# Optimization experiments

Measured on AMD Instinct MI355X. Metric: run time of the kernel, lower is better.

## Reference

```python
import jax, jax.numpy as jnp
import numpy as np

IN_DIM = 256
OUT_DIM = 256
GRID_SIZE = 8
K = 3  # spline_order
LOW, UP = -1.0, 1.0
BATCH = 512


def _control_grid():
    # equally spaced control points, extended by K on each side (paper sec 2.4)
    spacing = (UP - LOW) / GRID_SIZE
    g = jnp.arange(-K, GRID_SIZE + K + 1, dtype=jnp.float32) * spacing + LOW
    # buffer shape (out_dim, in_dim, G + 2K + 1)
    return jnp.broadcast_to(g[None, None, :], (OUT_DIM, IN_DIM, g.shape[0]))


def _bspline_bases(x, grid):
    # x: (B, in_dim); grid: (out, in, T). Cox-de Boor recursion.
    xx = x[:, None, :, None]          # (B, 1, in, 1)
    g = grid[None]                    # (1, out, in, T)
    # order-0 (piecewise-constant) bases
    b = ((xx >= g[..., :-1]) & (xx < g[..., 1:])).astype(x.dtype)
    for j in range(1, K + 1):
        b = (xx - g[..., :-(j + 1)]) / (g[..., j:-1] - g[..., :-(j + 1)]) * b[..., :-1] \
          + (g[..., j + 1:] - xx) / (g[..., j + 1:] - g[..., 1:-j]) * b[..., 1:]
    return b  # (B, out, in, G + K)


def setup_inputs() -> dict:
    key = jax.random.key(0)
    k1, k2, k3 = jax.random.split(key, 3)
    x = jax.random.normal(k1, (BATCH, IN_DIM), dtype=jnp.float32)
    # xavier_normal_ on (out, in, G+K): fan_in = in*(G+K) -> std = sqrt(2/(fan_in+fan_out))
    fan_out = IN_DIM * (GRID_SIZE + K)  # torch convention: dim0 = fan_out, rest = fan_in
    fan_in = OUT_DIM * (GRID_SIZE + K)
    std = float(np.sqrt(2.0 / (fan_in + fan_out)))
    coef = jax.random.normal(k2, (OUT_DIM, IN_DIM, GRID_SIZE + K), dtype=jnp.float32) * std
    residual_weight = jax.random.normal(k3, (OUT_DIM, IN_DIM), dtype=jnp.float32) * 0.1
    univariate_weight = jnp.ones((OUT_DIM, IN_DIM), dtype=jnp.float32)
    return {"x": x, "coef": coef, "residual_weight": residual_weight,
            "univariate_weight": univariate_weight}


def reference(x, coef, residual_weight, univariate_weight):
    grid = _control_grid()
    bases = _bspline_bases(x, grid)                      # (B, out, in, G+K)
    spline = jnp.einsum('boig,oig->boi', bases, coef)    # sum over grid dim
    phi = residual_weight[None, :, :] * jax.nn.silu(x)[:, None, :] \
        + univariate_weight[None, :, :] * spline          # (B, out, in)
    return jnp.sum(phi, axis=-1)                          # (B, out)
```

## Files before the change

kernel.cpp:

```cpp
#include <hip/hip_runtime.h>
#include <hip/hip_bf16.h>

typedef unsigned short ushort_t;
typedef unsigned int uint_t;
typedef __attribute__((ext_vector_type(8))) short short8;
typedef __attribute__((ext_vector_type(4))) float f32x4;

#define IN_DIM 256
#define OUT_DIM 256
#define BATCH 512
#define NSPL 11
#define KSLOT 12
#define KDIM (IN_DIM * KSLOT)
#define BKU 384
#define NCHUNK 8

__device__ __forceinline__ uint_t pk2(float lo, float hi) {
  __hip_bfloat162 h = __float22bfloat162_rn(make_float2(lo, hi));
  union { __hip_bfloat162 h2; uint_t u; } c; c.h2 = h;
  return c.u;
}

__global__ __launch_bounds__(256) void build_aw(const float* __restrict__ x,
                                                const float* __restrict__ coef,
                                                const float* __restrict__ rw,
                                                const float* __restrict__ uw,
                                                ushort_t* __restrict__ A,
                                                ushort_t* __restrict__ W) {
  __shared__ float rowc[IN_DIM * NSPL];
  const int bx = blockIdx.x;
  const int t = threadIdx.x;

  if (bx < BATCH) {
    const float xf = x[bx * IN_DIM + t];
    const float tt = (xf + 1.75f) * 4.0f;
    const float fJ = floorf(tt);
    const int J = (int)fJ;
    const float u = tt - fJ;
    const float u2 = u * u, u3 = u2 * u, um = 1.0f - u;
    const float n0 = um * um * um * (1.0f / 6.0f);
    const float n1 = 0.5f * u3 - u2 + (4.0f / 6.0f);
    const float n2 = -0.5f * u3 + 0.5f * u2 + 0.5f * u + (1.0f / 6.0f);
    const float n3 = u3 * (1.0f / 6.0f);
    const float silu = xf / (1.0f + __expf(-xf));

    float v[12];
#pragma unroll
    for (int g = 0; g < NSPL; ++g) {
      float val = 0.0f;
      val = (J == g + 3) ? n0 : val;
      val = (J == g + 2) ? n1 : val;
      val = (J == g + 1) ? n2 : val;
      val = (J == g    ) ? n3 : val;
      v[g] = val;
    }
    v[11] = silu;

    uint_t* dst = (uint_t*)(A + (size_t)bx * KDIM + t * KSLOT);
#pragma unroll
    for (int j = 0; j < 6; ++j) dst[j] = pk2(v[2 * j], v[2 * j + 1]);
  } else {
    const int o = bx - BATCH;
    const float* src = coef + (size_t)o * IN_DIM * NSPL;
#pragma unroll
    for (int j = 0; j < 11; ++j) rowc[t + j * 256] = src[t + j * 256];
    __syncthreads();

    const float us = uw[o * IN_DIM + t];
    const float r  = rw[o * IN_DIM + t];
    const float* c = &rowc[t * NSPL];
    uint_t* dst = (uint_t*)(W + (size_t)o * KDIM + t * KSLOT);
    dst[0] = pk2(us * c[0], us * c[1]);
    dst[1] = pk2(us * c[2], us * c[3]);
    dst[2] = pk2(us * c[4], us * c[5]);
    dst[3] = pk2(us * c[6], us * c[7]);
    dst[4] = pk2(us * c[8], us * c[9]);
    dst[5] = pk2(us * c[10], r);
  }
}

__global__ __launch_bounds__(256, 3) void gemm(const ushort_t* __restrict__ A,
                                               const ushort_t* __restrict__ W,
                                               float* __restrict__ out) {
  __shared__ __attribute__((aligned(16))) ushort_t As[2][16 * BKU];
  __shared__ __attribute__((aligned(16))) ushort_t Ws[2][16 * BKU];
  __shared__ f32x4 red[3][64];

  const int tid = threadIdx.x;
  const int lane = tid & 63;
  const int w = tid >> 6;
  const int B = blockIdx.x;
  const int mt = B >> 4;
  const int nt = ((B & 7) << 1) | ((B >> 3) & 1);
  const int b0 = mt * 16, o0 = nt * 16;
  const int mn = lane & 15;
  const int klane = (lane >> 4) * 8;

  int srcOff[3], ldsOff[3];
#pragma unroll
  for (int i = 0; i < 3; ++i) {
    const int F = ((w * 3 + i) * 64 + lane) * 8;
    const int rowi = F / BKU;
    const int coli = F % BKU;
    srcOff[i] = rowi * KDIM + coli;
    ldsOff[i] = rowi * BKU + (coli ^ ((rowi & 7) << 3));
  }
  const ushort_t* Ap = A + (size_t)b0 * KDIM;
  const ushort_t* Wp = W + (size_t)o0 * KDIM;

  const int mrow = mn * BKU;
  const int msw = (mn & 7) << 3;

  f32x4 acc = {0.f, 0.f, 0.f, 0.f};
  short8 sa0, sa1, sa2, sw0, sw1, sw2;

#define ISSUE(C)                                                              \
  {                                                                           \
    const int kb = (C) * BKU;                                                 \
    sa0 = *(const short8*)(Ap + srcOff[0] + kb);                              \
    sa1 = *(const short8*)(Ap + srcOff[1] + kb);                              \
    sa2 = *(const short8*)(Ap + srcOff[2] + kb);                              \
    sw0 = *(const short8*)(Wp + srcOff[0] + kb);                              \
    sw1 = *(const short8*)(Wp + srcOff[1] + kb);                              \
    sw2 = *(const short8*)(Wp + srcOff[2] + kb);                              \
  }

#define COMMIT(BUF)                                                           \
  {                                                                           \
    *(short8*)&As[BUF][ldsOff[0]] = sa0;                                      \
    *(short8*)&As[BUF][ldsOff[1]] = sa1;                                      \
    *(short8*)&As[BUF][ldsOff[2]] = sa2;                                      \
    *(short8*)&Ws[BUF][ldsOff[0]] = sw0;                                      \
    *(short8*)&Ws[BUF][ldsOff[1]] = sw1;                                      \
    *(short8*)&Ws[BUF][ldsOff[2]] = sw2;                                      \
  }

  ISSUE(0)
  COMMIT(0)
  __syncthreads();

  for (int c = 0; c < NCHUNK; ++c) {
    const int cur = c & 1;

    if (c + 1 < NCHUNK) { ISSUE(c + 1) }

#pragma unroll
    for (int q = 0; q < 3; ++q) {
      const int kidx = w * 96 + q * 32 + klane;
      const int idx = mrow + (kidx ^ msw);
      short8 af  = *(const short8*)&As[cur][idx];
      short8 bfr = *(const short8*)&Ws[cur][idx];
      acc = __builtin_amdgcn_mfma_f32_16x16x32_bf16(af, bfr, acc, 0, 0, 0);
    }

    if (c + 1 < NCHUNK) { COMMIT(cur ^ 1) }
    __syncthreads();
  }

  if (w > 0) red[w - 1][lane] = acc;
  __syncthreads();

  if (w == 0) {
    const f32x4 t0 = red[0][lane];
    const f32x4 t1 = red[1][lane];
    const f32x4 t2 = red[2][lane];
#pragma unroll
    for (int q = 0; q < 4; ++q) acc[q] += t0[q] + t1[q] + t2[q];

    const int col = o0 + mn;
    const int rbase = b0 + (lane >> 4) * 4;
#pragma unroll
    for (int r = 0; r < 4; ++r) {
      out[(size_t)(rbase + r) * OUT_DIM + col] = acc[r];
    }
  }
}

extern "C" void kernel_launch(void* const* d_in, const int* in_sizes, int n_in,
                              void* d_out, int out_size, void* d_ws, size_t ws_size,
                              hipStream_t stream) {
  const float* x    = (const float*)d_in[0];
  const float* coef = (const float*)d_in[1];
  const float* rw   = (const float*)d_in[2];
  const float* uw   = (const float*)d_in[3];
  float* out = (float*)d_out;

  ushort_t* A = (ushort_t*)d_ws;
  ushort_t* W = A + (size_t)BATCH * KDIM;

  build_aw<<<BATCH + OUT_DIM, 256, 0, stream>>>(x, coef, rw, uw, A, W);
  gemm<<<512, 256, 0, stream>>>(A, W, out);
}
```

Measured before the change: 17.86 us.

## Fuse B-spline basis construction into GEMM A-tile packing in LDS

Removes the global A matrix (spline bases plus SiLU per batch row). The GEMM kernel now reads x directly, evaluates the cubic B-spline weights and SiLU, and writes them swizzled into the shared-memory A tile. The W stream is double-buffered through two register sets with an unrolled two-phase loop. This saves a global write and read of the large bf16 A matrix, at the cost of recomputing bases in every column-tile block and extra scattered LDS stores. Out-of-range basis writes go to a dump area in the reduction buffer.

```diff
diff --git a/kernel.cpp b/kernel.cpp
--- a/kernel.cpp
+++ b/kernel.cpp
@@ -21,70 +21,70 @@
   return c.u;
 }
 
-__global__ __launch_bounds__(256) void build_aw(const float* __restrict__ x,
-                                                const float* __restrict__ coef,
-                                                const float* __restrict__ rw,
-                                                const float* __restrict__ uw,
-                                                ushort_t* __restrict__ A,
-                                                ushort_t* __restrict__ W) {
+__global__ __launch_bounds__(256) void build_w(const float* __restrict__ coef,
+                                               const float* __restrict__ rw,
+                                               const float* __restrict__ uw,
+                                               ushort_t* __restrict__ W) {
   __shared__ float rowc[IN_DIM * NSPL];
-  const int bx = blockIdx.x;
+  const int o = blockIdx.x;
   const int t = threadIdx.x;
 
-  if (bx < BATCH) {
-    const float xf = x[bx * IN_DIM + t];
-    const float tt = (xf + 1.75f) * 4.0f;
-    const float fJ = floorf(tt);
-    const int J = (int)fJ;
-    const float u = tt - fJ;
-    const float u2 = u * u, u3 = u2 * u, um = 1.0f - u;
-    const float n0 = um * um * um * (1.0f / 6.0f);
-    const float n1 = 0.5f * u3 - u2 + (4.0f / 6.0f);
-    const float n2 = -0.5f * u3 + 0.5f * u2 + 0.5f * u + (1.0f / 6.0f);
-    const float n3 = u3 * (1.0f / 6.0f);
-    const float silu = xf / (1.0f + __expf(-xf));
-
-    float v[12];
-#pragma unroll
-    for (int g = 0; g < NSPL; ++g) {
-      float val = 0.0f;
-      val = (J == g + 3) ? n0 : val;
-      val = (J == g + 2) ? n1 : val;
-      val = (J == g + 1) ? n2 : val;
-      val = (J == g    ) ? n3 : val;
-      v[g] = val;
-    }
-    v[11] = silu;
-
-    uint_t* dst = (uint_t*)(A + (size_t)bx * KDIM + t * KSLOT);
-#pragma unroll
-    for (int j = 0; j < 6; ++j) dst[j] = pk2(v[2 * j], v[2 * j + 1]);
-  } else {
-    const int o = bx - BATCH;
-    const float* src = coef + (size_t)o * IN_DIM * NSPL;
-#pragma unroll
-    for (int j = 0; j < 11; ++j) rowc[t + j * 256] = src[t + j * 256];
-    __syncthreads();
-
-    const float us = uw[o * IN_DIM + t];
-    const float r  = rw[o * IN_DIM + t];
-    const float* c = &rowc[t * NSPL];
-    uint_t* dst = (uint_t*)(W + (size_t)o * KDIM + t * KSLOT);
-    dst[0] = pk2(us * c[0], us * c[1]);
-    dst[1] = pk2(us * c[2], us * c[3]);
-    dst[2] = pk2(us * c[4], us * c[5]);
-    dst[3] = pk2(us * c[6], us * c[7]);
-    dst[4] = pk2(us * c[8], us * c[9]);
-    dst[5] = pk2(us * c[10], r);
-  }
-}
-
-__global__ __launch_bounds__(256, 3) void gemm(const ushort_t* __restrict__ A,
+  const float* src = coef + (size_t)o * IN_DIM * NSPL;
+#pragma unroll
+  for (int j = 0; j < 11; ++j) rowc[t + j * 256] = src[t + j * 256];
+  __syncthreads();
+
+  const float us = uw[o * IN_DIM + t];
+  const float r  = rw[o * IN_DIM + t];
+  const float* c = &rowc[t * NSPL];
+  uint_t* dst = (uint_t*)(W + (size_t)o * KDIM + t * KSLOT);
+  dst[0] = pk2(us * c[0], us * c[1]);
+  dst[1] = pk2(us * c[2], us * c[3]);
+  dst[2] = pk2(us * c[4], us * c[5]);
+  dst[3] = pk2(us * c[6], us * c[7]);
+  dst[4] = pk2(us * c[8], us * c[9]);
+  dst[5] = pk2(us * c[10], r);
+}
+
+__device__ __forceinline__ void packA_swz(ushort_t* rowbase, int cellu, int swz,
+                                          ushort_t* dumpp, float xf) {
+  const float t = (xf + 1.75f) * 4.0f;
+  const float fJ = floorf(t);
+  const int J = (int)fJ;
+  const float u = t - fJ;
+  const float u2 = u * u, u3 = u2 * u, um = 1.0f - u;
+  const float n0 = um * um * um * (1.0f / 6.0f);
+  const float n1 = 0.5f * u3 - u2 + (4.0f / 6.0f);
+  const float n2 = -0.5f * u3 + 0.5f * u2 + 0.5f * u + (1.0f / 6.0f);
+  const float n3 = u3 * (1.0f / 6.0f);
+  const float silu = xf / (1.0f + __expf(-xf));
+
+  *(unsigned long long*)&rowbase[(cellu + 0) ^ swz] = 0ull;
+  *(unsigned long long*)&rowbase[(cellu + 4) ^ swz] = 0ull;
+  *(unsigned long long*)&rowbase[(cellu + 8) ^ swz] = 0ull;
+
+  const uint_t p01 = pk2(n0, n1);
+  const uint_t p23 = pk2(n2, n3);
+  const uint_t psl = pk2(silu, silu);
+
+  const int base = J - 3;
+  ushort_t* w0 = ((unsigned)(base + 0) <= 10u) ? &rowbase[(cellu + base + 0) ^ swz] : (dumpp + 0);
+  ushort_t* w1 = ((unsigned)(base + 1) <= 10u) ? &rowbase[(cellu + base + 1) ^ swz] : (dumpp + 1);
+  ushort_t* w2 = ((unsigned)(base + 2) <= 10u) ? &rowbase[(cellu + base + 2) ^ swz] : (dumpp + 2);
+  ushort_t* w3 = ((unsigned)(base + 3) <= 10u) ? &rowbase[(cellu + base + 3) ^ swz] : (dumpp + 3);
+  *w0 = (ushort_t)p01;
+  *w1 = (ushort_t)(p01 >> 16);
+  *w2 = (ushort_t)p23;
+  *w3 = (ushort_t)(p23 >> 16);
+  rowbase[(cellu + 11) ^ swz] = (ushort_t)psl;
+}
+
+__global__ __launch_bounds__(256, 3) void gemm(const float* __restrict__ x,
                                                const ushort_t* __restrict__ W,
                                                float* __restrict__ out) {
   __shared__ __attribute__((aligned(16))) ushort_t As[2][16 * BKU];
   __shared__ __attribute__((aligned(16))) ushort_t Ws[2][16 * BKU];
-  __shared__ f32x4 red[3][64];
+  __shared__ __attribute__((aligned(16))) f32x4 red[3][64];
 
   const int tid = threadIdx.x;
   const int lane = tid & 63;
@@ -96,6 +96,18 @@
   const int mn = lane & 15;
   const int klane = (lane >> 4) * 8;
 
+  const int row = tid >> 4;
+  const int i0 = tid & 15;
+  const int aswz = (row & 7) << 3;
+
+  float xreg[16];
+  const float* xp = x + (size_t)(b0 + row) * IN_DIM;
+#pragma unroll
+  for (int c2 = 0; c2 < 8; ++c2) {
+    xreg[2 * c2]     = xp[32 * c2 + i0];
+    xreg[2 * c2 + 1] = xp[32 * c2 + i0 + 16];
+  }
+
   int srcOff[3], ldsOff[3];
 #pragma unroll
   for (int i = 0; i < 3; ++i) {
@@ -105,55 +117,60 @@
     srcOff[i] = rowi * KDIM + coli;
     ldsOff[i] = rowi * BKU + (coli ^ ((rowi & 7) << 3));
   }
-  const ushort_t* Ap = A + (size_t)b0 * KDIM;
   const ushort_t* Wp = W + (size_t)o0 * KDIM;
 
   const int mrow = mn * BKU;
   const int msw = (mn & 7) << 3;
 
   f32x4 acc = {0.f, 0.f, 0.f, 0.f};
-  short8 sa0, sa1, sa2, sw0, sw1, sw2;
-
-#define ISSUE(C)                                                              \
-  {                                                                           \
-    const int kb = (C) * BKU;                                                 \
-    sa0 = *(const short8*)(Ap + srcOff[0] + kb);                              \
-    sa1 = *(const short8*)(Ap + srcOff[1] + kb);                              \
-    sa2 = *(const short8*)(Ap + srcOff[2] + kb);                              \
-    sw0 = *(const short8*)(Wp + srcOff[0] + kb);                              \
-    sw1 = *(const short8*)(Wp + srcOff[1] + kb);                              \
-    sw2 = *(const short8*)(Wp + srcOff[2] + kb);                              \
-  }
-
-#define COMMIT(BUF)                                                           \
-  {                                                                           \
-    *(short8*)&As[BUF][ldsOff[0]] = sa0;                                      \
-    *(short8*)&As[BUF][ldsOff[1]] = sa1;                                      \
-    *(short8*)&As[BUF][ldsOff[2]] = sa2;                                      \
-    *(short8*)&Ws[BUF][ldsOff[0]] = sw0;                                      \
-    *(short8*)&Ws[BUF][ldsOff[1]] = sw1;                                      \
-    *(short8*)&Ws[BUF][ldsOff[2]] = sw2;                                      \
-  }
-
-  ISSUE(0)
-  COMMIT(0)
+  short8 sa0, sa1, sa2, sb0, sb1, sb2;
+
+#define ISSUE_A(C) { const int kb=(C)*BKU; \
+    sa0 = *(const short8*)(Wp+srcOff[0]+kb); \
+    sa1 = *(const short8*)(Wp+srcOff[1]+kb); \
+    sa2 = *(const short8*)(Wp+srcOff[2]+kb); }
+#define ISSUE_B(C) { const int kb=(C)*BKU; \
+    sb0 = *(const short8*)(Wp+srcOff[0]+kb); \
+    sb1 = *(const short8*)(Wp+srcOff[1]+kb); \
+    sb2 = *(const short8*)(Wp+srcOff[2]+kb); }
+#define COMMIT_A(BUF) { *(short8*)&Ws[BUF][ldsOff[0]] = sa0; \
+    *(short8*)&Ws[BUF][ldsOff[1]] = sa1; *(short8*)&Ws[BUF][ldsOff[2]] = sa2; }
+#define COMMIT_B(BUF) { *(short8*)&Ws[BUF][ldsOff[0]] = sb0; \
+    *(short8*)&Ws[BUF][ldsOff[1]] = sb1; *(short8*)&Ws[BUF][ldsOff[2]] = sb2; }
+
+#define APACK(C, BUF) { ushort_t* rb = &As[BUF][row * BKU]; \
+    ushort_t* dp = ((ushort_t*)red) + tid * 4; \
+    packA_swz(rb, i0 * KSLOT, aswz, dp, xreg[2 * (C)]); \
+    packA_swz(rb, (i0 + 16) * KSLOT, aswz, dp, xreg[2 * (C) + 1]); }
+
+#define MFMA3(BUF) { _Pragma("unroll") \
+    for (int q = 0; q < 3; ++q) { \
+      const int kidx = w * 96 + q * 32 + klane; \
+      const int idx = mrow + (kidx ^ msw); \
+      short8 af  = *(const short8*)&As[BUF][idx]; \
+      short8 bfr = *(const short8*)&Ws[BUF][idx]; \
+      acc = __builtin_amdgcn_mfma_f32_16x16x32_bf16(af, bfr, acc, 0, 0, 0); }}
+
+  ISSUE_A(0)
+  COMMIT_A(0)
+  APACK(0, 0)
+  ISSUE_B(1)
   __syncthreads();
 
-  for (int c = 0; c < NCHUNK; ++c) {
-    const int cur = c & 1;
-
-    if (c + 1 < NCHUNK) { ISSUE(c + 1) }
-
-#pragma unroll
-    for (int q = 0; q < 3; ++q) {
-      const int kidx = w * 96 + q * 32 + klane;
-      const int idx = mrow + (kidx ^ msw);
-      short8 af  = *(const short8*)&As[cur][idx];
-      short8 bfr = *(const short8*)&Ws[cur][idx];
-      acc = __builtin_amdgcn_mfma_f32_16x16x32_bf16(af, bfr, acc, 0, 0, 0);
+#pragma unroll
+  for (int cc = 0; cc < 4; ++cc) {
+    MFMA3(0)
+    if (cc < 3) { ISSUE_A(2 * cc + 2) }
+    APACK(2 * cc + 1, 1)
+    COMMIT_B(1)
+    __syncthreads();
+
+    MFMA3(1)
+    if (cc < 3) {
+      ISSUE_B(2 * cc + 3)
+      APACK(2 * cc + 2, 0)
+      COMMIT_A(0)
     }
-
-    if (c + 1 < NCHUNK) { COMMIT(cur ^ 1) }
     __syncthreads();
   }
 
@@ -185,9 +202,8 @@
   const float* uw   = (const float*)d_in[3];
   float* out = (float*)d_out;
 
-  ushort_t* A = (ushort_t*)d_ws;
-  ushort_t* W = A + (size_t)BATCH * KDIM;
-
-  build_aw<<<BATCH + OUT_DIM, 256, 0, stream>>>(x, coef, rw, uw, A, W);
-  gemm<<<512, 256, 0, stream>>>(A, W, out);
-}
+  ushort_t* W = (ushort_t*)d_ws;
+
+  build_w<<<OUT_DIM, 256, 0, stream>>>(coef, rw, uw, W);
+  gemm<<<512, 256, 0, stream>>>(x, W, out);
+}
```

Result: slower. 18.79 us (+5.2%).

## Use direct global-to-LDS loads with a triple-buffered pipeline and pre-swizzled operands

Applied to the files above, without the earlier changes.

The GEMM now loads its tiles with global_load_lds DMA straight into LDS, with no round trip through registers, and uses three LDS buffers so loads run two chunks ahead. Explicit vmcnt waits and raw barriers replace the per-iteration syncthreads. Because the DMA writes LDS linearly, build_aw now stores A and W with the XOR swizzle already applied in global memory. Occupancy drops from 3 to 2 blocks per CU because of the larger LDS footprint. The hand-written waitcnt counts are fragile and could break correctness if the compiler emits other memory operations.

```diff
diff --git a/kernel.cpp b/kernel.cpp
--- a/kernel.cpp
+++ b/kernel.cpp
@@ -19,6 +19,12 @@
   __hip_bfloat162 h = __float22bfloat162_rn(make_float2(lo, hi));
   union { __hip_bfloat162 h2; uint_t u; } c; c.h2 = h;
   return c.u;
+}
+
+__device__ __forceinline__ void gload16(const void* g, void* l) {
+  __builtin_amdgcn_global_load_lds(
+      (const __attribute__((address_space(1))) unsigned int*)g,
+      (__attribute__((address_space(3))) unsigned int*)l, 16, 0, 0);
 }
 
 __global__ __launch_bounds__(256) void build_aw(const float* __restrict__ x,
@@ -56,9 +62,11 @@
     }
     v[11] = silu;
 
-    uint_t* dst = (uint_t*)(A + (size_t)bx * KDIM + t * KSLOT);
-#pragma unroll
-    for (int j = 0; j < 6; ++j) dst[j] = pk2(v[2 * j], v[2 * j + 1]);
+    const int swz = (bx & 7) << 3;
+    uint_t* dstrow = (uint_t*)(A + (size_t)bx * KDIM);
+#pragma unroll
+    for (int j = 0; j < 6; ++j)
+      dstrow[((t * KSLOT + 2 * j) ^ swz) >> 1] = pk2(v[2 * j], v[2 * j + 1]);
   } else {
     const int o = bx - BATCH;
     const float* src = coef + (size_t)o * IN_DIM * NSPL;
@@ -69,21 +77,26 @@
     const float us = uw[o * IN_DIM + t];
     const float r  = rw[o * IN_DIM + t];
     const float* c = &rowc[t * NSPL];
-    uint_t* dst = (uint_t*)(W + (size_t)o * KDIM + t * KSLOT);
-    dst[0] = pk2(us * c[0], us * c[1]);
-    dst[1] = pk2(us * c[2], us * c[3]);
-    dst[2] = pk2(us * c[4], us * c[5]);
-    dst[3] = pk2(us * c[6], us * c[7]);
-    dst[4] = pk2(us * c[8], us * c[9]);
-    dst[5] = pk2(us * c[10], r);
-  }
-}
-
-__global__ __launch_bounds__(256, 3) void gemm(const ushort_t* __restrict__ A,
+    const int swz = (o & 7) << 3;
+    uint_t* dstrow = (uint_t*)(W + (size_t)o * KDIM);
+    uint_t pv[6];
+    pv[0] = pk2(us * c[0], us * c[1]);
+    pv[1] = pk2(us * c[2], us * c[3]);
+    pv[2] = pk2(us * c[4], us * c[5]);
+    pv[3] = pk2(us * c[6], us * c[7]);
+    pv[4] = pk2(us * c[8], us * c[9]);
+    pv[5] = pk2(us * c[10], r);
+#pragma unroll
+    for (int j = 0; j < 6; ++j)
+      dstrow[((t * KSLOT + 2 * j) ^ swz) >> 1] = pv[j];
+  }
+}
+
+__global__ __launch_bounds__(256, 2) void gemm(const ushort_t* __restrict__ A,
                                                const ushort_t* __restrict__ W,
                                                float* __restrict__ out) {
-  __shared__ __attribute__((aligned(16))) ushort_t As[2][16 * BKU];
-  __shared__ __attribute__((aligned(16))) ushort_t Ws[2][16 * BKU];
+  __shared__ __attribute__((aligned(16))) ushort_t As[3][16 * BKU];
+  __shared__ __attribute__((aligned(16))) ushort_t Ws[3][16 * BKU];
   __shared__ f32x4 red[3][64];
 
   const int tid = threadIdx.x;
@@ -96,14 +109,14 @@
   const int mn = lane & 15;
   const int klane = (lane >> 4) * 8;
 
-  int srcOff[3], ldsOff[3];
+  int srcOff[3], ldsBase[3];
 #pragma unroll
   for (int i = 0; i < 3; ++i) {
     const int F = ((w * 3 + i) * 64 + lane) * 8;
     const int rowi = F / BKU;
     const int coli = F % BKU;
     srcOff[i] = rowi * KDIM + coli;
-    ldsOff[i] = rowi * BKU + (coli ^ ((rowi & 7) << 3));
+    ldsBase[i] = (w * 3 + i) * 512;
   }
   const ushort_t* Ap = A + (size_t)b0 * KDIM;
   const ushort_t* Wp = W + (size_t)o0 * KDIM;
@@ -112,49 +125,46 @@
   const int msw = (mn & 7) << 3;
 
   f32x4 acc = {0.f, 0.f, 0.f, 0.f};
-  short8 sa0, sa1, sa2, sw0, sw1, sw2;
-
-#define ISSUE(C)                                                              \
-  {                                                                           \
+
+#define DMA6(C, BUF) {                                                        \
     const int kb = (C) * BKU;                                                 \
-    sa0 = *(const short8*)(Ap + srcOff[0] + kb);                              \
-    sa1 = *(const short8*)(Ap + srcOff[1] + kb);                              \
-    sa2 = *(const short8*)(Ap + srcOff[2] + kb);                              \
-    sw0 = *(const short8*)(Wp + srcOff[0] + kb);                              \
-    sw1 = *(const short8*)(Wp + srcOff[1] + kb);                              \
-    sw2 = *(const short8*)(Wp + srcOff[2] + kb);                              \
-  }
-
-#define COMMIT(BUF)                                                           \
-  {                                                                           \
-    *(short8*)&As[BUF][ldsOff[0]] = sa0;                                      \
-    *(short8*)&As[BUF][ldsOff[1]] = sa1;                                      \
-    *(short8*)&As[BUF][ldsOff[2]] = sa2;                                      \
-    *(short8*)&Ws[BUF][ldsOff[0]] = sw0;                                      \
-    *(short8*)&Ws[BUF][ldsOff[1]] = sw1;                                      \
-    *(short8*)&Ws[BUF][ldsOff[2]] = sw2;                                      \
-  }
-
-  ISSUE(0)
-  COMMIT(0)
-  __syncthreads();
-
-  for (int c = 0; c < NCHUNK; ++c) {
-    const int cur = c & 1;
-
-    if (c + 1 < NCHUNK) { ISSUE(c + 1) }
-
-#pragma unroll
-    for (int q = 0; q < 3; ++q) {
-      const int kidx = w * 96 + q * 32 + klane;
-      const int idx = mrow + (kidx ^ msw);
-      short8 af  = *(const short8*)&As[cur][idx];
-      short8 bfr = *(const short8*)&Ws[cur][idx];
-      acc = __builtin_amdgcn_mfma_f32_16x16x32_bf16(af, bfr, acc, 0, 0, 0);
-    }
-
-    if (c + 1 < NCHUNK) { COMMIT(cur ^ 1) }
-    __syncthreads();
+    gload16(Ap + srcOff[0] + kb, &As[BUF][ldsBase[0]]);                       \
+    gload16(Ap + srcOff[1] + kb, &As[BUF][ldsBase[1]]);                       \
+    gload16(Ap + srcOff[2] + kb, &As[BUF][ldsBase[2]]);                       \
+    gload16(Wp + srcOff[0] + kb, &Ws[BUF][ldsBase[0]]);                       \
+    gload16(Wp + srcOff[1] + kb, &Ws[BUF][ldsBase[1]]);                       \
+    gload16(Wp + srcOff[2] + kb, &Ws[BUF][ldsBase[2]]); }
+
+#define MFMA3(BUF) { _Pragma("unroll")                                        \
+    for (int q = 0; q < 3; ++q) {                                             \
+      const int kidx = w * 96 + q * 32 + klane;                               \
+      const int idx = mrow + (kidx ^ msw);                                    \
+      short8 af  = *(const short8*)&As[BUF][idx];                             \
+      short8 bfr = *(const short8*)&Ws[BUF][idx];                             \
+      acc = __builtin_amdgcn_mfma_f32_16x16x32_bf16(af, bfr, acc, 0, 0, 0); }}
+
+#define PHASE_W6(C, BUF, NBUF, DO_ISSUE) {                                    \
+    asm volatile("s_waitcnt vmcnt(6)" ::: "memory");                          \
+    __builtin_amdgcn_s_barrier();                                             \
+    __builtin_amdgcn_sched_barrier(0);                                        \
+    if (DO_ISSUE) DMA6((C) + 2, NBUF)                                         \
+    MFMA3(BUF) }
+
+  DMA6(0, 0)
+  DMA6(1, 1)
+
+  PHASE_W6(0, 0, 2, 1)
+  PHASE_W6(1, 1, 0, 1)
+  PHASE_W6(2, 2, 1, 1)
+  PHASE_W6(3, 0, 2, 1)
+  PHASE_W6(4, 1, 0, 1)
+  PHASE_W6(5, 2, 1, 1)
+  PHASE_W6(6, 0, 0, 0)
+  {
+    asm volatile("s_waitcnt vmcnt(0)" ::: "memory");
+    __builtin_amdgcn_s_barrier();
+    __builtin_amdgcn_sched_barrier(0);
+    MFMA3(1)
   }
 
   if (w > 0) red[w - 1][lane] = acc;
```

Result: slower. 19.02 us (+6.5%).
